# Optimization experiments

Measured on AMD Instinct MI355X. Metric: run time of the kernel, lower is better.

## Reference

```python
import jax, jax.numpy as jnp
import numpy as np
from jax import lax

T, N, F, H, E = 8, 20000, 128, 256, 320000
LEAK = 0.9


def setup_inputs() -> dict:
    key = jax.random.key(0)
    k = jax.random.split(key, 7)
    x = jax.random.normal(k[0], (T, N, F), dtype=jnp.float32)
    edge_index = jax.random.randint(k[1], (2, E), 0, N, dtype=jnp.int32)
    # reservoir weights, scaled ~1/sqrt(fan_in) so tanh stays in its active range
    w_in0 = jax.random.normal(k[2], (H, F), dtype=jnp.float32) / jnp.sqrt(F)
    w_rec0 = jax.random.normal(k[3], (H, H), dtype=jnp.float32) / jnp.sqrt(H)
    w_in1 = jax.random.normal(k[4], (H, H), dtype=jnp.float32) / jnp.sqrt(H)
    w_rec1 = jax.random.normal(k[5], (H, H), dtype=jnp.float32) / jnp.sqrt(H)
    leakage = jnp.array(LEAK, dtype=jnp.float32)
    return {"x": x, "edge_index": edge_index, "w_in0": w_in0, "w_rec0": w_rec0,
            "w_in1": w_in1, "w_rec1": w_rec1, "leakage": leakage}


def reference(x, edge_index, w_in0, w_rec0, w_in1, w_rec1, leakage):
    # DynamicGraphReservoir with 2 ReservoirConvLayers, fixed graph over time,
    # zero initial states, no pooling, fully=False, return_sequences=False.
    src, dst = edge_index[0], edge_index[1]
    num_nodes = x.shape[1]

    def layer(w_in, w_rec, inp, state):
        # neighbour aggregation: sum_{(j->i) in E} state[j]   (scatter-add)
        agg = jax.ops.segment_sum(state[src], dst, num_segments=num_nodes)
        return leakage * jnp.tanh(inp @ w_in.T + agg @ w_rec.T) + (1.0 - leakage) * state

    def step(states, xt):
        s0, s1 = states
        s0 = layer(w_in0, w_rec0, xt, s0)   # layer 0 consumes input signal
        s1 = layer(w_in1, w_rec1, s0, s1)   # layer 1 consumes layer-0 state
        return (s0, s1), None

    init = (jnp.zeros((num_nodes, w_rec0.shape[0]), x.dtype),
            jnp.zeros((num_nodes, w_rec1.shape[0]), x.dtype))
    (s0, s1), _ = lax.scan(step, init, x)
    return s1  # final-layer final state: (nodes, hidden)
```

## Files before the change

### kernel.cpp

```cpp
#include <hip/hip_runtime.h>
#include <math.h>

#define T_STEPS 8
#define N_NODES 20000
#define F_IN    128
#define H_DIM   256
#define E_EDGES 320000

typedef __attribute__((ext_vector_type(8))) short short8;
typedef __attribute__((ext_vector_type(4))) float f32x4;

__device__ __forceinline__ void split2(float v, unsigned short& h, unsigned short& l) {
    unsigned vi = __float_as_uint(v);
    h = (unsigned short)(vi >> 16);
    float hf = __uint_as_float(vi & 0xffff0000u);
    l = (unsigned short)(__float_as_uint(v - hf) >> 16);
}


__global__ void count_kernel(const int* __restrict__ dst, int* __restrict__ counts, int E) {
    int e = blockIdx.x * blockDim.x + threadIdx.x;
    if (e < E) atomicAdd(&counts[dst[e]], 1);
}

__global__ void scan_kernel(const int* __restrict__ counts, int* __restrict__ row_ptr,
                            int* __restrict__ cursors, int n) {
    __shared__ int buf[1024];
    __shared__ int carry_s;
    int tid = threadIdx.x;
    if (tid == 0) carry_s = 0;
    __syncthreads();
    for (int base = 0; base < n; base += 1024) {
        int i = base + tid;
        int v = (i < n) ? counts[i] : 0;
        buf[tid] = v;
        __syncthreads();
        for (int off = 1; off < 1024; off <<= 1) {
            int t = (tid >= off) ? buf[tid - off] : 0;
            __syncthreads();
            buf[tid] += t;
            __syncthreads();
        }
        int incl = buf[tid];
        int carry = carry_s;
        if (i < n) {
            int ex = carry + incl - v;
            row_ptr[i] = ex;
            cursors[i] = ex;
        }
        __syncthreads();
        if (tid == 1023) carry_s = carry + incl;
        __syncthreads();
    }
    if (tid == 0) row_ptr[n] = carry_s;
}

__global__ void fill_kernel(const int* __restrict__ src, const int* __restrict__ dst,
                            int* __restrict__ cursors, int* __restrict__ col, int E) {
    int e = blockIdx.x * blockDim.x + threadIdx.x;
    if (e < E) {
        int d = dst[e];
        int p = atomicAdd(&cursors[d], 1);
        col[p] = src[e];
    }
}


__global__ void cvt_frag(const float* __restrict__ W, int K,
                         unsigned short* __restrict__ fh, unsigned short* __restrict__ fl) {
    int g = blockIdx.x * 256 + threadIdx.x;
    int KP32 = K >> 5;
    int total = (H_DIM / 16) * KP32 * 64;
    if (g >= total) return;
    int lane = g & 63;
    int kp = (g >> 6) % KP32;
    int rt = g / (KP32 << 6);
    int r = rt * 16 + (lane & 15);
    int c = kp * 32 + (lane >> 4) * 8;
    const float* p = W + (size_t)r * K + c;
    short8 h, l;
    #pragma unroll
    for (int j = 0; j < 8; ++j) {
        unsigned short hh, ll;
        split2(p[j], hh, ll);
        h[j] = (short)hh; l[j] = (short)ll;
    }
    *(short8*)(fh + (size_t)g * 8) = h;
    *(short8*)(fl + (size_t)g * 8) = l;
}


__global__ __launch_bounds__(256) void fused_update(
        const float* __restrict__ A1, int K1,
        const float* __restrict__ s_prev,
        const unsigned short* __restrict__ B1h, const unsigned short* __restrict__ B1l,
        const unsigned short* __restrict__ B2h, const unsigned short* __restrict__ B2l,
        float* __restrict__ s_new,
        const int* __restrict__ row_ptr, const int* __restrict__ col,
        const float* __restrict__ leak_ptr, int do_gather) {
    __shared__ float aggs[32][260];
    const int tid = threadIdx.x;
    const int lane = tid & 63, w = tid >> 6;
    const int fr = lane & 15, fq = lane >> 4;
    const int m0 = blockIdx.x * 32;
    const int wn = w * 64;
    const int rtbase = w * 4;

    if (do_gather) {
        const float4* s4 = (const float4*)s_prev;
        #pragma unroll 1
        for (int i = 0; i < 8; ++i) {
            int r = w * 8 + i;
            int beg = row_ptr[m0 + r], end = row_ptr[m0 + r + 1];
            float x0 = 0.f, y0 = 0.f, z0 = 0.f, w0 = 0.f;
            float x1 = 0.f, y1 = 0.f, z1 = 0.f, w1 = 0.f;
            float x2 = 0.f, y2 = 0.f, z2 = 0.f, w2 = 0.f;
            float x3 = 0.f, y3 = 0.f, z3 = 0.f, w3 = 0.f;
            int j = beg;
            for (; j + 3 < end; j += 4) {
                int c0 = col[j], c1 = col[j + 1], c2 = col[j + 2], c3 = col[j + 3];
                float4 v0 = s4[(size_t)c0 * 64 + lane];
                float4 v1 = s4[(size_t)c1 * 64 + lane];
                float4 v2 = s4[(size_t)c2 * 64 + lane];
                float4 v3 = s4[(size_t)c3 * 64 + lane];
                x0 += v0.x; y0 += v0.y; z0 += v0.z; w0 += v0.w;
                x1 += v1.x; y1 += v1.y; z1 += v1.z; w1 += v1.w;
                x2 += v2.x; y2 += v2.y; z2 += v2.z; w2 += v2.w;
                x3 += v3.x; y3 += v3.y; z3 += v3.z; w3 += v3.w;
            }
            for (; j < end; ++j) {
                float4 v = s4[(size_t)col[j] * 64 + lane];
                x0 += v.x; y0 += v.y; z0 += v.z; w0 += v.w;
            }
            float4 t;
            t.x = (x0 + x1) + (x2 + x3);
            t.y = (y0 + y1) + (y2 + y3);
            t.z = (z0 + z1) + (z2 + z3);
            t.w = (w0 + w1) + (w2 + w3);
            *(float4*)&aggs[r][lane * 4] = t;
        }
        __syncthreads();
    }

    f32x4 acc[2][4];
    #pragma unroll
    for (int mi = 0; mi < 2; ++mi)
        #pragma unroll
        for (int nt = 0; nt < 4; ++nt)
            acc[mi][nt] = (f32x4){0.f, 0.f, 0.f, 0.f};

    {
        const int KP32 = K1 >> 5;
        #pragma unroll 1
        for (int kp = 0; kp < KP32; ++kp) {
            short8 ah[2], al[2];
            #pragma unroll
            for (int mi = 0; mi < 2; ++mi) {
                const float* ap = A1 + (size_t)(m0 + mi * 16 + fr) * K1 + kp * 32 + fq * 8;
                float4 v0 = *(const float4*)ap;
                float4 v1 = *(const float4*)(ap + 4);
                unsigned short h, l;
                split2(v0.x, h, l); ah[mi][0] = (short)h; al[mi][0] = (short)l;
                split2(v0.y, h, l); ah[mi][1] = (short)h; al[mi][1] = (short)l;
                split2(v0.z, h, l); ah[mi][2] = (short)h; al[mi][2] = (short)l;
                split2(v0.w, h, l); ah[mi][3] = (short)h; al[mi][3] = (short)l;
                split2(v1.x, h, l); ah[mi][4] = (short)h; al[mi][4] = (short)l;
                split2(v1.y, h, l); ah[mi][5] = (short)h; al[mi][5] = (short)l;
                split2(v1.z, h, l); ah[mi][6] = (short)h; al[mi][6] = (short)l;
                split2(v1.w, h, l); ah[mi][7] = (short)h; al[mi][7] = (short)l;
            }
            short8 bh[4], bl[4];
            #pragma unroll
            for (int nt = 0; nt < 4; ++nt) {
                size_t off = ((size_t)((rtbase + nt) * KP32 + kp) * 64 + lane) * 8;
                bh[nt] = *(const short8*)(B1h + off);
                bl[nt] = *(const short8*)(B1l + off);
            }
            #pragma unroll
            for (int mi = 0; mi < 2; ++mi)
                #pragma unroll
                for (int nt = 0; nt < 4; ++nt) {
                    f32x4 c = acc[mi][nt];
                    c = __builtin_amdgcn_mfma_f32_16x16x32_bf16(ah[mi], bh[nt], c, 0, 0, 0);
                    c = __builtin_amdgcn_mfma_f32_16x16x32_bf16(al[mi], bh[nt], c, 0, 0, 0);
                    c = __builtin_amdgcn_mfma_f32_16x16x32_bf16(ah[mi], bl[nt], c, 0, 0, 0);
                    acc[mi][nt] = c;
                }
        }
    }

    if (B2h) {
        #pragma unroll 1
        for (int kp = 0; kp < 8; ++kp) {
            short8 ah[2], al[2];
            #pragma unroll
            for (int mi = 0; mi < 2; ++mi) {
                const float* ap = &aggs[mi * 16 + fr][kp * 32 + fq * 8];
                float4 v0 = *(const float4*)ap;
                float4 v1 = *(const float4*)(ap + 4);
                unsigned short h, l;
                split2(v0.x, h, l); ah[mi][0] = (short)h; al[mi][0] = (short)l;
                split2(v0.y, h, l); ah[mi][1] = (short)h; al[mi][1] = (short)l;
                split2(v0.z, h, l); ah[mi][2] = (short)h; al[mi][2] = (short)l;
                split2(v0.w, h, l); ah[mi][3] = (short)h; al[mi][3] = (short)l;
                split2(v1.x, h, l); ah[mi][4] = (short)h; al[mi][4] = (short)l;
                split2(v1.y, h, l); ah[mi][5] = (short)h; al[mi][5] = (short)l;
                split2(v1.z, h, l); ah[mi][6] = (short)h; al[mi][6] = (short)l;
                split2(v1.w, h, l); ah[mi][7] = (short)h; al[mi][7] = (short)l;
            }
            short8 bh[4], bl[4];
            #pragma unroll
            for (int nt = 0; nt < 4; ++nt) {
                size_t off = ((size_t)((rtbase + nt) * 8 + kp) * 64 + lane) * 8;
                bh[nt] = *(const short8*)(B2h + off);
                bl[nt] = *(const short8*)(B2l + off);
            }
            #pragma unroll
            for (int mi = 0; mi < 2; ++mi)
                #pragma unroll
                for (int nt = 0; nt < 4; ++nt) {
                    f32x4 c = acc[mi][nt];
                    c = __builtin_amdgcn_mfma_f32_16x16x32_bf16(ah[mi], bh[nt], c, 0, 0, 0);
                    c = __builtin_amdgcn_mfma_f32_16x16x32_bf16(al[mi], bh[nt], c, 0, 0, 0);
                    c = __builtin_amdgcn_mfma_f32_16x16x32_bf16(ah[mi], bl[nt], c, 0, 0, 0);
                    acc[mi][nt] = c;
                }
        }
    }

    const float leak = leak_ptr[0], il = 1.0f - leak;
    #pragma unroll
    for (int mi = 0; mi < 2; ++mi)
        #pragma unroll
        for (int r = 0; r < 4; ++r) {
            int m = m0 + mi * 16 + fq * 4 + r;
            #pragma unroll
            for (int nt = 0; nt < 4; ++nt) {
                int n = wn + nt * 16 + fr;
                size_t idx = (size_t)m * H_DIM + n;
                float old = s_prev[idx];
                float pre = acc[mi][nt][r];
                float e = __expf(2.0f * pre);
                float th = 1.0f - 2.0f / (e + 1.0f);
                s_new[idx] = leak * th + il * old;
            }
        }
}


extern "C" void kernel_launch(void* const* d_in, const int* in_sizes, int n_in,
                              void* d_out, int out_size, void* d_ws, size_t ws_size,
                              hipStream_t stream) {
    const float* x        = (const float*)d_in[0];
    const int*   edge     = (const int*)d_in[1];
    const float* w_in0    = (const float*)d_in[2];
    const float* w_rec0   = (const float*)d_in[3];
    const float* w_in1    = (const float*)d_in[4];
    const float* w_rec1   = (const float*)d_in[5];
    const float* leak_ptr = (const float*)d_in[6];

    const int* src = edge;
    const int* dst = edge + E_EDGES;

    char* ws = (char*)d_ws;
    size_t off = 0;
    auto alloc = [&](size_t bytes) -> char* {
        char* p = ws + off;
        off += (bytes + 255) & ~(size_t)255;
        return p;
    };
    const size_t state_bytes = (size_t)N_NODES * H_DIM * sizeof(float);
    float* s0b[2]; float* s1b[2];
    s0b[0] = (float*)alloc(state_bytes);
    s0b[1] = (float*)alloc(state_bytes);
    s1b[0] = (float*)d_out;
    s1b[1] = (float*)alloc(state_bytes);
    unsigned short* w0h  = (unsigned short*)alloc(256 * 128 * 2);
    unsigned short* w0l  = (unsigned short*)alloc(256 * 128 * 2);
    unsigned short* wr0h = (unsigned short*)alloc(256 * 256 * 2);
    unsigned short* wr0l = (unsigned short*)alloc(256 * 256 * 2);
    unsigned short* w1h  = (unsigned short*)alloc(256 * 256 * 2);
    unsigned short* w1l  = (unsigned short*)alloc(256 * 256 * 2);
    unsigned short* wr1h = (unsigned short*)alloc(256 * 256 * 2);
    unsigned short* wr1l = (unsigned short*)alloc(256 * 256 * 2);
    int* row_ptr = (int*)alloc((N_NODES + 1) * sizeof(int));
    int* cursors = (int*)alloc(N_NODES * sizeof(int));
    int* counts  = (int*)alloc(N_NODES * sizeof(int));
    int* col     = (int*)alloc((size_t)E_EDGES * sizeof(int));

    hipMemsetAsync(s0b[0], 0, state_bytes, stream);
    hipMemsetAsync(s1b[0], 0, state_bytes, stream);
    hipMemsetAsync(counts, 0, N_NODES * sizeof(int), stream);

    cvt_frag<<<16, 256, 0, stream>>>(w_in0, F_IN, w0h, w0l);
    cvt_frag<<<32, 256, 0, stream>>>(w_rec0, H_DIM, wr0h, wr0l);
    cvt_frag<<<32, 256, 0, stream>>>(w_in1, H_DIM, w1h, w1l);
    cvt_frag<<<32, 256, 0, stream>>>(w_rec1, H_DIM, wr1h, wr1l);

    count_kernel<<<(E_EDGES + 255) / 256, 256, 0, stream>>>(dst, counts, E_EDGES);
    scan_kernel<<<1, 1024, 0, stream>>>(counts, row_ptr, cursors, N_NODES);
    fill_kernel<<<(E_EDGES + 255) / 256, 256, 0, stream>>>(src, dst, cursors, col, E_EDGES);

    dim3 ugrid(N_NODES / 32);

    for (int t = 0; t < T_STEPS; ++t) {
        const float* xt = x + (size_t)t * N_NODES * F_IN;
        int rd = t & 1, wr = rd ^ 1;
        int dg = (t > 0) ? 1 : 0;
        fused_update<<<ugrid, 256, 0, stream>>>(
            xt, F_IN, s0b[rd],
            w0h, w0l, dg ? wr0h : nullptr, dg ? wr0l : nullptr,
            s0b[wr], row_ptr, col, leak_ptr, dg);
        fused_update<<<ugrid, 256, 0, stream>>>(
            s0b[wr], H_DIM, s1b[rd],
            w1h, w1l, dg ? wr1h : nullptr, dg ? wr1l : nullptr,
            s1b[wr], row_ptr, col, leak_ptr, dg);
    }
}
```

Baseline: 1.265 ms.

## Halve rows per block to 16 and deepen gather unroll to 8 edges

Each fused_update block now handles 16 node rows instead of 32, which doubles the grid to 1250 blocks and halves the shared aggregation buffer and accumulator registers. The aim is more blocks in flight across the CUs and higher occupancy to hide the latency of the irregular neighbour gather. The gather loop also unrolls 8 edges at a time with eight float4 accumulators, putting more independent loads in flight. In exchange, each B-fragment load now feeds only one M tile, so weight-fragment traffic per output row doubles.

```diff
diff --git a/kernel.cpp b/kernel.cpp
--- a/kernel.cpp
+++ b/kernel.cpp
@@ -98,153 +98,150 @@
         float* __restrict__ s_new,
         const int* __restrict__ row_ptr, const int* __restrict__ col,
         const float* __restrict__ leak_ptr, int do_gather) {
-    __shared__ float aggs[32][260];
+    __shared__ float aggs[16][260];
     const int tid = threadIdx.x;
     const int lane = tid & 63, w = tid >> 6;
     const int fr = lane & 15, fq = lane >> 4;
-    const int m0 = blockIdx.x * 32;
+    const int m0 = blockIdx.x * 16;
     const int wn = w * 64;
     const int rtbase = w * 4;
 
     if (do_gather) {
         const float4* s4 = (const float4*)s_prev;
         #pragma unroll 1
-        for (int i = 0; i < 8; ++i) {
-            int r = w * 8 + i;
+        for (int i = 0; i < 4; ++i) {
+            int r = w * 4 + i;
             int beg = row_ptr[m0 + r], end = row_ptr[m0 + r + 1];
-            float x0 = 0.f, y0 = 0.f, z0 = 0.f, w0 = 0.f;
-            float x1 = 0.f, y1 = 0.f, z1 = 0.f, w1 = 0.f;
-            float x2 = 0.f, y2 = 0.f, z2 = 0.f, w2 = 0.f;
-            float x3 = 0.f, y3 = 0.f, z3 = 0.f, w3 = 0.f;
+            float4 a0 = {0,0,0,0}, a1 = {0,0,0,0}, a2 = {0,0,0,0}, a3 = {0,0,0,0};
+            float4 a4 = {0,0,0,0}, a5 = {0,0,0,0}, a6 = {0,0,0,0}, a7 = {0,0,0,0};
             int j = beg;
+            for (; j + 7 < end; j += 8) {
+                float4 v0 = s4[(size_t)col[j    ] * 64 + lane];
+                float4 v1 = s4[(size_t)col[j + 1] * 64 + lane];
+                float4 v2 = s4[(size_t)col[j + 2] * 64 + lane];
+                float4 v3 = s4[(size_t)col[j + 3] * 64 + lane];
+                float4 v4 = s4[(size_t)col[j + 4] * 64 + lane];
+                float4 v5 = s4[(size_t)col[j + 5] * 64 + lane];
+                float4 v6 = s4[(size_t)col[j + 6] * 64 + lane];
+                float4 v7 = s4[(size_t)col[j + 7] * 64 + lane];
+                a0.x += v0.x; a0.y += v0.y; a0.z += v0.z; a0.w += v0.w;
+                a1.x += v1.x; a1.y += v1.y; a1.z += v1.z; a1.w += v1.w;
+                a2.x += v2.x; a2.y += v2.y; a2.z += v2.z; a2.w += v2.w;
+                a3.x += v3.x; a3.y += v3.y; a3.z += v3.z; a3.w += v3.w;
+                a4.x += v4.x; a4.y += v4.y; a4.z += v4.z; a4.w += v4.w;
+                a5.x += v5.x; a5.y += v5.y; a5.z += v5.z; a5.w += v5.w;
+                a6.x += v6.x; a6.y += v6.y; a6.z += v6.z; a6.w += v6.w;
+                a7.x += v7.x; a7.y += v7.y; a7.z += v7.z; a7.w += v7.w;
+            }
             for (; j + 3 < end; j += 4) {
-                int c0 = col[j], c1 = col[j + 1], c2 = col[j + 2], c3 = col[j + 3];
-                float4 v0 = s4[(size_t)c0 * 64 + lane];
-                float4 v1 = s4[(size_t)c1 * 64 + lane];
-                float4 v2 = s4[(size_t)c2 * 64 + lane];
-                float4 v3 = s4[(size_t)c3 * 64 + lane];
-                x0 += v0.x; y0 += v0.y; z0 += v0.z; w0 += v0.w;
-                x1 += v1.x; y1 += v1.y; z1 += v1.z; w1 += v1.w;
-                x2 += v2.x; y2 += v2.y; z2 += v2.z; w2 += v2.w;
-                x3 += v3.x; y3 += v3.y; z3 += v3.z; w3 += v3.w;
+                float4 v0 = s4[(size_t)col[j    ] * 64 + lane];
+                float4 v1 = s4[(size_t)col[j + 1] * 64 + lane];
+                float4 v2 = s4[(size_t)col[j + 2] * 64 + lane];
+                float4 v3 = s4[(size_t)col[j + 3] * 64 + lane];
+                a0.x += v0.x; a0.y += v0.y; a0.z += v0.z; a0.w += v0.w;
+                a1.x += v1.x; a1.y += v1.y; a1.z += v1.z; a1.w += v1.w;
+                a2.x += v2.x; a2.y += v2.y; a2.z += v2.z; a2.w += v2.w;
+                a3.x += v3.x; a3.y += v3.y; a3.z += v3.z; a3.w += v3.w;
             }
             for (; j < end; ++j) {
                 float4 v = s4[(size_t)col[j] * 64 + lane];
-                x0 += v.x; y0 += v.y; z0 += v.z; w0 += v.w;
+                a0.x += v.x; a0.y += v.y; a0.z += v.z; a0.w += v.w;
             }
             float4 t;
-            t.x = (x0 + x1) + (x2 + x3);
-            t.y = (y0 + y1) + (y2 + y3);
-            t.z = (z0 + z1) + (z2 + z3);
-            t.w = (w0 + w1) + (w2 + w3);
+            t.x = ((a0.x + a1.x) + (a2.x + a3.x)) + ((a4.x + a5.x) + (a6.x + a7.x));
+            t.y = ((a0.y + a1.y) + (a2.y + a3.y)) + ((a4.y + a5.y) + (a6.y + a7.y));
+            t.z = ((a0.z + a1.z) + (a2.z + a3.z)) + ((a4.z + a5.z) + (a6.z + a7.z));
+            t.w = ((a0.w + a1.w) + (a2.w + a3.w)) + ((a4.w + a5.w) + (a6.w + a7.w));
             *(float4*)&aggs[r][lane * 4] = t;
         }
         __syncthreads();
     }
 
-    f32x4 acc[2][4];
+    f32x4 acc[4];
     #pragma unroll
-    for (int mi = 0; mi < 2; ++mi)
-        #pragma unroll
-        for (int nt = 0; nt < 4; ++nt)
-            acc[mi][nt] = (f32x4){0.f, 0.f, 0.f, 0.f};
+    for (int nt = 0; nt < 4; ++nt)
+        acc[nt] = (f32x4){0.f, 0.f, 0.f, 0.f};
 
     {
         const int KP32 = K1 >> 5;
         #pragma unroll 1
         for (int kp = 0; kp < KP32; ++kp) {
-            short8 ah[2], al[2];
-            #pragma unroll
-            for (int mi = 0; mi < 2; ++mi) {
-                const float* ap = A1 + (size_t)(m0 + mi * 16 + fr) * K1 + kp * 32 + fq * 8;
+            short8 ah, al;
+            {
+                const float* ap = A1 + (size_t)(m0 + fr) * K1 + kp * 32 + fq * 8;
                 float4 v0 = *(const float4*)ap;
                 float4 v1 = *(const float4*)(ap + 4);
                 unsigned short h, l;
-                split2(v0.x, h, l); ah[mi][0] = (short)h; al[mi][0] = (short)l;
-                split2(v0.y, h, l); ah[mi][1] = (short)h; al[mi][1] = (short)l;
-                split2(v0.z, h, l); ah[mi][2] = (short)h; al[mi][2] = (short)l;
-                split2(v0.w, h, l); ah[mi][3] = (short)h; al[mi][3] = (short)l;
-                split2(v1.x, h, l); ah[mi][4] = (short)h; al[mi][4] = (short)l;
-                split2(v1.y, h, l); ah[mi][5] = (short)h; al[mi][5] = (short)l;
-                split2(v1.z, h, l); ah[mi][6] = (short)h; al[mi][6] = (short)l;
-                split2(v1.w, h, l); ah[mi][7] = (short)h; al[mi][7] = (short)l;
-            }
-            short8 bh[4], bl[4];
+                split2(v0.x, h, l); ah[0] = (short)h; al[0] = (short)l;
+                split2(v0.y, h, l); ah[1] = (short)h; al[1] = (short)l;
+                split2(v0.z, h, l); ah[2] = (short)h; al[2] = (short)l;
+                split2(v0.w, h, l); ah[3] = (short)h; al[3] = (short)l;
+                split2(v1.x, h, l); ah[4] = (short)h; al[4] = (short)l;
+                split2(v1.y, h, l); ah[5] = (short)h; al[5] = (short)l;
+                split2(v1.z, h, l); ah[6] = (short)h; al[6] = (short)l;
+                split2(v1.w, h, l); ah[7] = (short)h; al[7] = (short)l;
+            }
             #pragma unroll
             for (int nt = 0; nt < 4; ++nt) {
                 size_t off = ((size_t)((rtbase + nt) * KP32 + kp) * 64 + lane) * 8;
-                bh[nt] = *(const short8*)(B1h + off);
-                bl[nt] = *(const short8*)(B1l + off);
-            }
-            #pragma unroll
-            for (int mi = 0; mi < 2; ++mi)
-                #pragma unroll
-                for (int nt = 0; nt < 4; ++nt) {
-                    f32x4 c = acc[mi][nt];
-                    c = __builtin_amdgcn_mfma_f32_16x16x32_bf16(ah[mi], bh[nt], c, 0, 0, 0);
-                    c = __builtin_amdgcn_mfma_f32_16x16x32_bf16(al[mi], bh[nt], c, 0, 0, 0);
-                    c = __builtin_amdgcn_mfma_f32_16x16x32_bf16(ah[mi], bl[nt], c, 0, 0, 0);
-                    acc[mi][nt] = c;
-                }
+                short8 bh = *(const short8*)(B1h + off);
+                short8 bl = *(const short8*)(B1l + off);
+                f32x4 c = acc[nt];
+                c = __builtin_amdgcn_mfma_f32_16x16x32_bf16(ah, bh, c, 0, 0, 0);
+                c = __builtin_amdgcn_mfma_f32_16x16x32_bf16(al, bh, c, 0, 0, 0);
+                c = __builtin_amdgcn_mfma_f32_16x16x32_bf16(ah, bl, c, 0, 0, 0);
+                acc[nt] = c;
+            }
         }
     }
 
     if (B2h) {
         #pragma unroll 1
         for (int kp = 0; kp < 8; ++kp) {
-            short8 ah[2], al[2];
-            #pragma unroll
-            for (int mi = 0; mi < 2; ++mi) {
-                const float* ap = &aggs[mi * 16 + fr][kp * 32 + fq * 8];
+            short8 ah, al;
+            {
+                const float* ap = &aggs[fr][kp * 32 + fq * 8];
                 float4 v0 = *(const float4*)ap;
                 float4 v1 = *(const float4*)(ap + 4);
                 unsigned short h, l;
-                split2(v0.x, h, l); ah[mi][0] = (short)h; al[mi][0] = (short)l;
-                split2(v0.y, h, l); ah[mi][1] = (short)h; al[mi][1] = (short)l;
-                split2(v0.z, h, l); ah[mi][2] = (short)h; al[mi][2] = (short)l;
-                split2(v0.w, h, l); ah[mi][3] = (short)h; al[mi][3] = (short)l;
-                split2(v1.x, h, l); ah[mi][4] = (short)h; al[mi][4] = (short)l;
-                split2(v1.y, h, l); ah[mi][5] = (short)h; al[mi][5] = (short)l;
-                split2(v1.z, h, l); ah[mi][6] = (short)h; al[mi][6] = (short)l;
-                split2(v1.w, h, l); ah[mi][7] = (short)h; al[mi][7] = (short)l;
-            }
-            short8 bh[4], bl[4];
+                split2(v0.x, h, l); ah[0] = (short)h; al[0] = (short)l;
+                split2(v0.y, h, l); ah[1] = (short)h; al[1] = (short)l;
+                split2(v0.z, h, l); ah[2] = (short)h; al[2] = (short)l;
+                split2(v0.w, h, l); ah[3] = (short)h; al[3] = (short)l;
+                split2(v1.x, h, l); ah[4] = (short)h; al[4] = (short)l;
+                split2(v1.y, h, l); ah[5] = (short)h; al[5] = (short)l;
+                split2(v1.z, h, l); ah[6] = (short)h; al[6] = (short)l;
+                split2(v1.w, h, l); ah[7] = (short)h; al[7] = (short)l;
+            }
             #pragma unroll
             for (int nt = 0; nt < 4; ++nt) {
                 size_t off = ((size_t)((rtbase + nt) * 8 + kp) * 64 + lane) * 8;
-                bh[nt] = *(const short8*)(B2h + off);
-                bl[nt] = *(const short8*)(B2l + off);
-            }
-            #pragma unroll
-            for (int mi = 0; mi < 2; ++mi)
-                #pragma unroll
-                for (int nt = 0; nt < 4; ++nt) {
-                    f32x4 c = acc[mi][nt];
-                    c = __builtin_amdgcn_mfma_f32_16x16x32_bf16(ah[mi], bh[nt], c, 0, 0, 0);
-                    c = __builtin_amdgcn_mfma_f32_16x16x32_bf16(al[mi], bh[nt], c, 0, 0, 0);
-                    c = __builtin_amdgcn_mfma_f32_16x16x32_bf16(ah[mi], bl[nt], c, 0, 0, 0);
-                    acc[mi][nt] = c;
-                }
+                short8 bh = *(const short8*)(B2h + off);
+                short8 bl = *(const short8*)(B2l + off);
+                f32x4 c = acc[nt];
+                c = __builtin_amdgcn_mfma_f32_16x16x32_bf16(ah, bh, c, 0, 0, 0);
+                c = __builtin_amdgcn_mfma_f32_16x16x32_bf16(al, bh, c, 0, 0, 0);
+                c = __builtin_amdgcn_mfma_f32_16x16x32_bf16(ah, bl, c, 0, 0, 0);
+                acc[nt] = c;
+            }
         }
     }
 
     const float leak = leak_ptr[0], il = 1.0f - leak;
     #pragma unroll
-    for (int mi = 0; mi < 2; ++mi)
+    for (int r = 0; r < 4; ++r) {
+        int m = m0 + fq * 4 + r;
         #pragma unroll
-        for (int r = 0; r < 4; ++r) {
-            int m = m0 + mi * 16 + fq * 4 + r;
-            #pragma unroll
-            for (int nt = 0; nt < 4; ++nt) {
-                int n = wn + nt * 16 + fr;
-                size_t idx = (size_t)m * H_DIM + n;
-                float old = s_prev[idx];
-                float pre = acc[mi][nt][r];
-                float e = __expf(2.0f * pre);
-                float th = 1.0f - 2.0f / (e + 1.0f);
-                s_new[idx] = leak * th + il * old;
-            }
-        }
+        for (int nt = 0; nt < 4; ++nt) {
+            int n = wn + nt * 16 + fr;
+            size_t idx = (size_t)m * H_DIM + n;
+            float old = s_prev[idx];
+            float pre = acc[nt][r];
+            float e = __expf(2.0f * pre);
+            float th = 1.0f - 2.0f / (e + 1.0f);
+            s_new[idx] = leak * th + il * old;
+        }
+    }
 }
 
 
@@ -301,7 +298,7 @@
     scan_kernel<<<1, 1024, 0, stream>>>(counts, row_ptr, cursors, N_NODES);
     fill_kernel<<<(E_EDGES + 255) / 256, 256, 0, stream>>>(src, dst, cursors, col, E_EDGES);
 
-    dim3 ugrid(N_NODES / 32);
+    dim3 ugrid(N_NODES / 16);
 
     for (int t = 0; t < T_STEPS; ++t) {
         const float* xt = x + (size_t)t * N_NODES * F_IN;
```

Result: slower. 1.500 ms (+18.5%).
